# Kernel optimization log

Hardware: AMD Instinct MI355X
Metric: run time of the kernel (lower is better)

## Reference

```python
import jax, jax.numpy as jnp
import numpy as np

NUM_HEADS = 16
HEAD_DIM = 64  # hidden 1024 / 16


def setup_inputs() -> dict:
    key = jax.random.key(0)
    k1, k2, k3 = jax.random.split(key, 3)
    B, S, H = 2, 2048, 1024
    return {
        "hidden_states": jax.random.normal(k1, (B, S, H), dtype=jnp.float32),
        "attention_mask": jnp.zeros((B, 1, 1, S), dtype=jnp.float32),
        "c_attn_w": jax.random.normal(k2, (H, 3 * H), dtype=jnp.float32) * 0.02,
        "c_attn_b": jnp.zeros((3 * H,), dtype=jnp.float32),
        "c_proj_w": jax.random.normal(k3, (H, H), dtype=jnp.float32) * 0.02,
        "c_proj_b": jnp.zeros((H,), dtype=jnp.float32),
    }


def reference(hidden_states, attention_mask, c_attn_w, c_attn_b, c_proj_w, c_proj_b):
    B, S, H = hidden_states.shape
    nH, hd = NUM_HEADS, HEAD_DIM
    # Conv1D: x @ w + b (HF weight layout is (in, out))
    qkv = hidden_states @ c_attn_w + c_attn_b  # [B,S,3H]
    q, k, v = jnp.split(qkv, 3, axis=-1)
    # split heads -> [B,nH,S,hd]
    def heads(t):
        return t.reshape(B, S, nH, hd).transpose(0, 2, 1, 3)
    q, k, v = heads(q), heads(k), heads(v)
    scores = jnp.einsum("bhqd,bhkd->bhqk", q, k) / np.sqrt(hd).astype(jnp.float32)
    scores = scores + attention_mask  # additive mask, broadcast [B,1,1,S]
    attn = jax.nn.softmax(scores, axis=-1)  # dropout is identity (eval)
    ctx = jnp.einsum("bhqk,bhkd->bhqd", attn, v)
    ctx = ctx.transpose(0, 2, 1, 3).reshape(B, S, H)  # merge heads
    out = ctx @ c_proj_w + c_proj_b
    return out
```

## Files before the change

kernel.cpp:

```cpp
#include <hip/hip_runtime.h>
#include <hip/hip_bf16.h>

typedef __attribute__((ext_vector_type(8))) short short8;
typedef __attribute__((ext_vector_type(4))) short short4v;
typedef __attribute__((ext_vector_type(4))) float f32x4;

__device__ __forceinline__ unsigned short f2bf(float f) {
  union { __hip_bfloat16 h; unsigned short u; } cv;
  cv.h = __float2bfloat16(f);
  return cv.u;
}

__device__ __forceinline__ void gld16(const void* g, void* l) {
  __builtin_amdgcn_global_load_lds(
      (const __attribute__((address_space(1))) unsigned int*)g,
      (__attribute__((address_space(3))) unsigned int*)l, 16, 0, 0);
}

__device__ __forceinline__ f32x4 mfma_bf16(short8 a, short8 b, f32x4 c) {
  return __builtin_amdgcn_mfma_f32_16x16x32_bf16(a, b, c, 0, 0, 0);
}

#define QSCALE 0.18033688011112042f
#define L2E    1.4426950408889634f

__global__ void prep(const float* __restrict__ x, unsigned short* __restrict__ xbf,
                     const float* __restrict__ wa, unsigned short* __restrict__ da,
                     const float* __restrict__ wp, unsigned short* __restrict__ dp) {
  __shared__ float tile[64][65];
  const int t = threadIdx.x;
  const int bid = blockIdx.x;
  if (bid < 4096) {
    int i = bid * 256 + t;
    float4 v = ((const float4*)x)[i];
    ushort4 o;
    o.x = f2bf(v.x); o.y = f2bf(v.y); o.z = f2bf(v.z); o.w = f2bf(v.w);
    ((ushort4*)xbf)[i] = o;
    return;
  }
  int idx = bid - 4096;
  const int tr = idx & 15;
  int y = idx >> 4;
  const float* src;
  unsigned short* dst;
  int C;
  if (y < 48) { src = wa; dst = da; C = 3072; }
  else        { src = wp; dst = dp; C = 1024; y -= 48; }
  const int tc = y;
#pragma unroll
  for (int i = 0; i < 16; ++i) {
    int id2 = t + i * 256;
    int lr = id2 >> 6, lc = id2 & 63;
    tile[lr][lc] = src[(size_t)(tr * 64 + lr) * C + tc * 64 + lc];
  }
  __syncthreads();
#pragma unroll
  for (int i = 0; i < 16; ++i) {
    int id2 = t + i * 256;
    int lr = id2 >> 6, lc = id2 & 63;
    dst[(size_t)(tc * 64 + lr) * 1024 + tr * 64 + lc] = f2bf(tile[lc][lr]);
  }
}

template <int KDIM>
__device__ __forceinline__ void gemm_core(const short* __restrict__ A, const short* __restrict__ Bt,
                                          int mbase, int nbase, short* As, short* Bs,
                                          int wm, int wn, int quad, int l16, int t,
                                          f32x4 (&acc)[4][4]) {
  for (int kt = 0; kt < KDIM / 32; ++kt) {
#pragma unroll
    for (int i = 0; i < 2; ++i) {
      int c = t + i * 256;
      int row = c >> 2, c4 = c & 3;
      gld16(A + (size_t)(mbase + row) * KDIM + kt * 32 + c4 * 8, (char*)As + c * 16);
      gld16(Bt + (size_t)(nbase + row) * KDIM + kt * 32 + c4 * 8, (char*)Bs + c * 16);
    }
    __syncthreads();
    short8 af[4], bf[4];
#pragma unroll
    for (int m = 0; m < 4; ++m)
      af[m] = *(const short8*)((const char*)As + (wm + m * 16 + l16) * 64 + quad * 16);
#pragma unroll
    for (int n = 0; n < 4; ++n)
      bf[n] = *(const short8*)((const char*)Bs + (wn + n * 16 + l16) * 64 + quad * 16);
#pragma unroll
    for (int m = 0; m < 4; ++m)
#pragma unroll
      for (int n = 0; n < 4; ++n)
        acc[m][n] = mfma_bf16(af[m], bf[n], acc[m][n]);
    __syncthreads();
  }
}

__global__ __launch_bounds__(256, 2) void gemm_qkv(
    const short* __restrict__ A, const short* __restrict__ Bt, const float* __restrict__ bias,
    unsigned short* __restrict__ q, unsigned short* __restrict__ k,
    unsigned short* __restrict__ vt) {
  __shared__ __align__(16) char smem[17408];
  short* As = (short*)smem;
  short* Bs = (short*)(smem + 8192);
  unsigned short* vlds = (unsigned short*)smem;
  const int t = threadIdx.x;
  const int wave = t >> 6, lane = t & 63;
  const int quad = lane >> 4, l16 = lane & 15;
  const int wm = (wave >> 1) * 64, wn = (wave & 1) * 64;
  const int mbase = blockIdx.x * 128, nbase = blockIdx.y * 128;
  f32x4 acc[4][4];
#pragma unroll
  for (int i = 0; i < 4; ++i)
#pragma unroll
    for (int j = 0; j < 4; ++j) acc[i][j] = (f32x4)0.0f;
  gemm_core<1024>(A, Bt, mbase, nbase, As, Bs, wm, wn, quad, l16, t, acc);

  if (nbase < 2048) {
#pragma unroll
    for (int n = 0; n < 4; ++n) {
      int col = nbase + wn + n * 16 + l16;
      float bc = bias[col];
      int which = col >> 10, rem = col & 1023;
      int h = rem >> 6, d = rem & 63;
      unsigned short* dst = which ? k : q;
      float scale = which ? 1.0f : QSCALE;
#pragma unroll
      for (int m = 0; m < 4; ++m) {
#pragma unroll
        for (int r = 0; r < 4; ++r) {
          int row = mbase + wm + m * 16 + quad * 4 + r;
          int b = row >> 11, s = row & 2047;
          dst[(((size_t)(b * 16 + h)) * 2048 + s) * 64 + d] = f2bf((acc[m][n][r] + bc) * scale);
        }
      }
    }
  } else {
    const int b = mbase >> 11, s0 = mbase & 2047;
    const int vcb = nbase - 2048;
    __syncthreads();
#pragma unroll
    for (int half = 0; half < 2; ++half) {
      if (wn == half * 64) {
#pragma unroll
        for (int n = 0; n < 4; ++n) {
          int col_l = n * 16 + l16;
          float bc = bias[nbase + half * 64 + col_l];
#pragma unroll
          for (int m = 0; m < 4; ++m)
#pragma unroll
            for (int r = 0; r < 4; ++r) {
              int row_l = wm + m * 16 + quad * 4 + r;
              int idx = (row_l & 64) + (row_l & 15) * 4 + ((row_l >> 4) & 3);
              vlds[col_l * 136 + idx] = f2bf(acc[m][n][r] + bc);
            }
        }
      }
      __syncthreads();
      int h = (vcb + half * 64) >> 6;
      size_t obase = ((size_t)(b * 16 + h)) * 64 * 2048;
#pragma unroll
      for (int i = 0; i < 4; ++i) {
        int c = t + i * 256;
        int d_l = c >> 4, c16 = c & 15;
        short8 v = *(const short8*)&vlds[d_l * 136 + c16 * 8];
        *(short8*)&vt[obase + (size_t)d_l * 2048 + s0 + c16 * 8] = v;
      }
      __syncthreads();
    }
  }
}

__global__ __launch_bounds__(256, 2) void gemm_proj(
    const short* __restrict__ A, const short* __restrict__ Bt, const float* __restrict__ bias,
    float* __restrict__ out) {
  __shared__ __align__(16) short As[64 * 32];
  __shared__ __align__(16) short Bs[128 * 32];
  const int t = threadIdx.x;
  const int wave = t >> 6, lane = t & 63;
  const int quad = lane >> 4, l16 = lane & 15;
  const int wm = (wave >> 1) * 32, wn = (wave & 1) * 64;
  const int mbase = blockIdx.x * 64, nbase = blockIdx.y * 128;
  f32x4 acc[2][4];
#pragma unroll
  for (int i = 0; i < 2; ++i)
#pragma unroll
    for (int j = 0; j < 4; ++j) acc[i][j] = (f32x4)0.0f;
  for (int kt = 0; kt < 32; ++kt) {
    {
      int row = t >> 2, c4 = t & 3;
      gld16(A + (size_t)(mbase + row) * 1024 + kt * 32 + c4 * 8, (char*)As + t * 16);
    }
#pragma unroll
    for (int i = 0; i < 2; ++i) {
      int c = t + i * 256;
      int row = c >> 2, c4 = c & 3;
      gld16(Bt + (size_t)(nbase + row) * 1024 + kt * 32 + c4 * 8, (char*)Bs + c * 16);
    }
    __syncthreads();
    short8 af[2], bf[4];
#pragma unroll
    for (int m = 0; m < 2; ++m)
      af[m] = *(const short8*)((const char*)As + (wm + m * 16 + l16) * 64 + quad * 16);
#pragma unroll
    for (int n = 0; n < 4; ++n)
      bf[n] = *(const short8*)((const char*)Bs + (wn + n * 16 + l16) * 64 + quad * 16);
#pragma unroll
    for (int m = 0; m < 2; ++m)
#pragma unroll
      for (int n = 0; n < 4; ++n)
        acc[m][n] = mfma_bf16(af[m], bf[n], acc[m][n]);
    __syncthreads();
  }
#pragma unroll
  for (int n = 0; n < 4; ++n) {
    int col = nbase + wn + n * 16 + l16;
    float bc = bias[col];
#pragma unroll
    for (int m = 0; m < 2; ++m)
#pragma unroll
      for (int r = 0; r < 4; ++r) {
        int row = mbase + wm + m * 16 + quad * 4 + r;
        out[(size_t)row * 1024 + col] = acc[m][n][r] + bc;
      }
  }
}

__global__ __launch_bounds__(256, 4) void flash_attn(
    const short* __restrict__ Qg, const short* __restrict__ Kg, const short* __restrict__ Vtg,
    const float* __restrict__ mask, unsigned short* __restrict__ ctx) {
  __shared__ __align__(16) unsigned char smem[40960];
  short* Psm = (short*)(smem + 32768);
  const int t = threadIdx.x;
  const int wave = t >> 6, lane = t & 63;
  const int quad = lane >> 4, l16 = lane & 15;
  const int bh = blockIdx.x, b = bh >> 4, h = bh & 15;
  const int qbase = blockIdx.y * 64;
  const size_t bh_off = (size_t)bh * 2048 * 64;

#pragma unroll
  for (int i = 0; i < 2; ++i) {
    int c = t + i * 256;
    int row = c >> 3, col = c & 7;
    gld16(Qg + bh_off + (size_t)(qbase + row) * 64 + (col ^ (row & 7)) * 8,
          (char*)smem + c * 16);
  }
  __syncthreads();
  short8 qf[2];
#pragma unroll
  for (int ks = 0; ks < 2; ++ks) {
    int row = wave * 16 + l16;
    qf[ks] = *(const short8*)((const char*)smem +
                              (row * 8 + ((ks * 4 + quad) ^ (l16 & 7))) * 16);
  }
  __syncthreads();

  auto stage = [&](int kn) {
    char* kd = (char*)smem + (kn & 1) * 8192;
    char* vd = (char*)smem + 16384 + (kn & 1) * 8192;
#pragma unroll
    for (int i = 0; i < 2; ++i) {
      int c = t + i * 256;
      int row = c >> 3, col = c & 7;
      gld16(Kg + bh_off + (size_t)(kn * 64 + row) * 64 + (col ^ (row & 7)) * 8,
            kd + c * 16);
      gld16(Vtg + ((size_t)bh * 64 + row) * 2048 + kn * 64 + (col ^ (row & 7)) * 8,
            vd + c * 16);
    }
  };

  f32x4 O[4];
  float l_i[4];
#pragma unroll
  for (int d = 0; d < 4; ++d) O[d] = (f32x4)0.0f;
#pragma unroll
  for (int r = 0; r < 4; ++r) l_i[r] = 0.0f;

  stage(0);
  __syncthreads();

  for (int kt = 0; kt < 32; ++kt) {
    const char* Kc = (const char*)smem + (kt & 1) * 8192;
    const char* Vc = (const char*)smem + 16384 + (kt & 1) * 8192;

    float mv[4];
#pragma unroll
    for (int n = 0; n < 4; ++n) mv[n] = mask[b * 2048 + kt * 64 + n * 16 + l16];

    if (kt < 31) stage(kt + 1);

    f32x4 sa[4];
#pragma unroll
    for (int n = 0; n < 4; ++n) sa[n] = (f32x4)0.0f;
    __builtin_amdgcn_s_setprio(1);
#pragma unroll
    for (int ks = 0; ks < 2; ++ks) {
#pragma unroll
      for (int n = 0; n < 4; ++n) {
        int row = n * 16 + l16;
        short8 kf = *(const short8*)(Kc + (row * 8 + ((ks * 4 + quad) ^ (l16 & 7))) * 16);
        sa[n] = mfma_bf16(qf[ks], kf, sa[n]);
      }
    }
    __builtin_amdgcn_s_setprio(0);

#pragma unroll
    for (int r = 0; r < 4; ++r) {
      float rs = 0.0f;
      short4v p4;
#pragma unroll
      for (int n = 0; n < 4; ++n) {
        float p = __builtin_amdgcn_exp2f(__builtin_fmaf(mv[n], L2E, sa[n][r]));
        rs += p;
        p4[n] = (short)f2bf(p);
      }
      int prow = wave * 16 + quad * 4 + r;
      *(short4v*)((char*)Psm + prow * 128 +
                  (((l16 >> 1) ^ (prow & 7)) * 16) + (l16 & 1) * 8) = p4;
      l_i[r] += rs;
    }
    asm volatile("" ::: "memory");

    __builtin_amdgcn_s_setprio(1);
#pragma unroll
    for (int ks = 0; ks < 2; ++ks) {
      int u = ks * 4 + quad;
      int prow = wave * 16 + l16;
      short8 pf = *(const short8*)((const char*)Psm + prow * 128 + ((u ^ (l16 & 7)) * 16));
#pragma unroll
      for (int db = 0; db < 4; ++db) {
        int d = db * 16 + l16;
        short8 vf = *(const short8*)(Vc + d * 128 + ((u ^ (d & 7)) * 16));
        O[db] = mfma_bf16(pf, vf, O[db]);
      }
    }
    __builtin_amdgcn_s_setprio(0);

    __syncthreads();
  }

#pragma unroll
  for (int r = 0; r < 4; ++r) {
    float l = l_i[r];
    l += __shfl_xor(l, 1);
    l += __shfl_xor(l, 2);
    l += __shfl_xor(l, 4);
    l += __shfl_xor(l, 8);
    float inv = 1.0f / l;
    int s = qbase + wave * 16 + quad * 4 + r;
    size_t o = ((size_t)b * 2048 + s) * 1024 + h * 64;
#pragma unroll
    for (int db = 0; db < 4; ++db)
      ctx[o + db * 16 + l16] = f2bf(O[db][r] * inv);
  }
}

extern "C" void kernel_launch(void* const* d_in, const int* in_sizes, int n_in,
                              void* d_out, int out_size, void* d_ws, size_t ws_size,
                              hipStream_t stream) {
  const float* x      = (const float*)d_in[0];
  const float* mask   = (const float*)d_in[1];
  const float* w_attn = (const float*)d_in[2];
  const float* b_attn = (const float*)d_in[3];
  const float* w_proj = (const float*)d_in[4];
  const float* b_proj = (const float*)d_in[5];
  float* out = (float*)d_out;

  char* ws = (char*)d_ws;
  const size_t MB = 1024 * 1024;
  short*          Xbf    = (short*)(ws);
  short*          Wqkv_t = (short*)(ws + 8 * MB);
  short*          Wprj_t = (short*)(ws + 14 * MB);
  unsigned short* Qb     = (unsigned short*)(ws + 16 * MB);
  unsigned short* Kb     = (unsigned short*)(ws + 24 * MB);
  unsigned short* Vtb    = (unsigned short*)(ws + 32 * MB);
  unsigned short* ctx    = (unsigned short*)Xbf;

  prep<<<5120, 256, 0, stream>>>(x, (unsigned short*)Xbf,
                                 w_attn, (unsigned short*)Wqkv_t,
                                 w_proj, (unsigned short*)Wprj_t);
  gemm_qkv<<<dim3(32, 24), 256, 0, stream>>>(Xbf, Wqkv_t, b_attn, Qb, Kb, Vtb);
  flash_attn<<<dim3(32, 32), 256, 0, stream>>>((const short*)Qb, (const short*)Kb,
                                               (const short*)Vtb, mask, ctx);
  gemm_proj<<<dim3(64, 8), 256, 0, stream>>>((const short*)ctx, Wprj_t, b_proj, out);
}
```

Baseline: 188.7 us.

## Process 128 query rows per flash-attention block to reuse K/V tiles

Each flash-attention block now handles 128 query rows instead of 64, with every wave computing two 16-row MFMA fragments. Each K and V fragment loaded from LDS then feeds two MFMAs, and the grid is halved, so each K/V tile is fetched from global memory half as often. In exchange the block uses more registers and more LDS (48KB), launch bounds drop occupancy to 2 blocks per CU, and only 512 blocks are launched, which gives less latency hiding.

```diff
diff --git a/kernel.cpp b/kernel.cpp
--- a/kernel.cpp
+++ b/kernel.cpp
@@ -222,33 +222,35 @@
   }
 }
 
-__global__ __launch_bounds__(256, 4) void flash_attn(
+__global__ __launch_bounds__(256, 2) void flash_attn(
     const short* __restrict__ Qg, const short* __restrict__ Kg, const short* __restrict__ Vtg,
     const float* __restrict__ mask, unsigned short* __restrict__ ctx) {
-  __shared__ __align__(16) unsigned char smem[40960];
+  __shared__ __align__(16) unsigned char smem[49152];
   short* Psm = (short*)(smem + 32768);
   const int t = threadIdx.x;
   const int wave = t >> 6, lane = t & 63;
   const int quad = lane >> 4, l16 = lane & 15;
   const int bh = blockIdx.x, b = bh >> 4, h = bh & 15;
-  const int qbase = blockIdx.y * 64;
+  const int qbase = blockIdx.y * 128;
   const size_t bh_off = (size_t)bh * 2048 * 64;
 
 #pragma unroll
-  for (int i = 0; i < 2; ++i) {
+  for (int i = 0; i < 4; ++i) {
     int c = t + i * 256;
     int row = c >> 3, col = c & 7;
     gld16(Qg + bh_off + (size_t)(qbase + row) * 64 + (col ^ (row & 7)) * 8,
           (char*)smem + c * 16);
   }
   __syncthreads();
-  short8 qf[2];
-#pragma unroll
-  for (int ks = 0; ks < 2; ++ks) {
-    int row = wave * 16 + l16;
-    qf[ks] = *(const short8*)((const char*)smem +
-                              (row * 8 + ((ks * 4 + quad) ^ (l16 & 7))) * 16);
-  }
+  short8 qf[2][2];
+#pragma unroll
+  for (int mf = 0; mf < 2; ++mf)
+#pragma unroll
+    for (int ks = 0; ks < 2; ++ks) {
+      int row = wave * 32 + mf * 16 + l16;
+      qf[mf][ks] = *(const short8*)((const char*)smem +
+                                    (row * 8 + ((ks * 4 + quad) ^ (l16 & 7))) * 16);
+    }
   __syncthreads();
 
   auto stage = [&](int kn) {
@@ -265,12 +267,16 @@
     }
   };
 
-  f32x4 O[4];
-  float l_i[4];
-#pragma unroll
-  for (int d = 0; d < 4; ++d) O[d] = (f32x4)0.0f;
-#pragma unroll
-  for (int r = 0; r < 4; ++r) l_i[r] = 0.0f;
+  f32x4 O[2][4];
+  float l_i[2][4];
+#pragma unroll
+  for (int mf = 0; mf < 2; ++mf)
+#pragma unroll
+    for (int d = 0; d < 4; ++d) O[mf][d] = (f32x4)0.0f;
+#pragma unroll
+  for (int mf = 0; mf < 2; ++mf)
+#pragma unroll
+    for (int r = 0; r < 4; ++r) l_i[mf][r] = 0.0f;
 
   stage(0);
   __syncthreads();
@@ -285,9 +291,11 @@
 
     if (kt < 31) stage(kt + 1);
 
-    f32x4 sa[4];
-#pragma unroll
-    for (int n = 0; n < 4; ++n) sa[n] = (f32x4)0.0f;
+    f32x4 sa[2][4];
+#pragma unroll
+    for (int mf = 0; mf < 2; ++mf)
+#pragma unroll
+      for (int n = 0; n < 4; ++n) sa[mf][n] = (f32x4)0.0f;
     __builtin_amdgcn_s_setprio(1);
 #pragma unroll
     for (int ks = 0; ks < 2; ++ks) {
@@ -295,25 +303,29 @@
       for (int n = 0; n < 4; ++n) {
         int row = n * 16 + l16;
         short8 kf = *(const short8*)(Kc + (row * 8 + ((ks * 4 + quad) ^ (l16 & 7))) * 16);
-        sa[n] = mfma_bf16(qf[ks], kf, sa[n]);
+        sa[0][n] = mfma_bf16(qf[0][ks], kf, sa[0][n]);
+        sa[1][n] = mfma_bf16(qf[1][ks], kf, sa[1][n]);
       }
     }
     __builtin_amdgcn_s_setprio(0);
 
 #pragma unroll
-    for (int r = 0; r < 4; ++r) {
-      float rs = 0.0f;
-      short4v p4;
-#pragma unroll
-      for (int n = 0; n < 4; ++n) {
-        float p = __builtin_amdgcn_exp2f(__builtin_fmaf(mv[n], L2E, sa[n][r]));
-        rs += p;
-        p4[n] = (short)f2bf(p);
-      }
-      int prow = wave * 16 + quad * 4 + r;
-      *(short4v*)((char*)Psm + prow * 128 +
-                  (((l16 >> 1) ^ (prow & 7)) * 16) + (l16 & 1) * 8) = p4;
-      l_i[r] += rs;
+    for (int mf = 0; mf < 2; ++mf) {
+#pragma unroll
+      for (int r = 0; r < 4; ++r) {
+        float rs = 0.0f;
+        short4v p4;
+#pragma unroll
+        for (int n = 0; n < 4; ++n) {
+          float p = __builtin_amdgcn_exp2f(__builtin_fmaf(mv[n], L2E, sa[mf][n][r]));
+          rs += p;
+          p4[n] = (short)f2bf(p);
+        }
+        int prow = wave * 32 + mf * 16 + quad * 4 + r;
+        *(short4v*)((char*)Psm + prow * 128 +
+                    (((l16 >> 1) ^ (prow & 7)) * 16) + (l16 & 1) * 8) = p4;
+        l_i[mf][r] += rs;
+      }
     }
     asm volatile("" ::: "memory");
 
@@ -321,13 +333,19 @@
 #pragma unroll
     for (int ks = 0; ks < 2; ++ks) {
       int u = ks * 4 + quad;
-      int prow = wave * 16 + l16;
-      short8 pf = *(const short8*)((const char*)Psm + prow * 128 + ((u ^ (l16 & 7)) * 16));
+      short8 vf[4];
 #pragma unroll
       for (int db = 0; db < 4; ++db) {
         int d = db * 16 + l16;
-        short8 vf = *(const short8*)(Vc + d * 128 + ((u ^ (d & 7)) * 16));
-        O[db] = mfma_bf16(pf, vf, O[db]);
+        vf[db] = *(const short8*)(Vc + d * 128 + ((u ^ (d & 7)) * 16));
+      }
+#pragma unroll
+      for (int mf = 0; mf < 2; ++mf) {
+        int prow = wave * 32 + mf * 16 + l16;
+        short8 pf = *(const short8*)((const char*)Psm + prow * 128 + ((u ^ (l16 & 7)) * 16));
+#pragma unroll
+        for (int db = 0; db < 4; ++db)
+          O[mf][db] = mfma_bf16(pf, vf[db], O[mf][db]);
       }
     }
     __builtin_amdgcn_s_setprio(0);
@@ -336,18 +354,21 @@
   }
 
 #pragma unroll
-  for (int r = 0; r < 4; ++r) {
-    float l = l_i[r];
-    l += __shfl_xor(l, 1);
-    l += __shfl_xor(l, 2);
-    l += __shfl_xor(l, 4);
-    l += __shfl_xor(l, 8);
-    float inv = 1.0f / l;
-    int s = qbase + wave * 16 + quad * 4 + r;
-    size_t o = ((size_t)b * 2048 + s) * 1024 + h * 64;
-#pragma unroll
-    for (int db = 0; db < 4; ++db)
-      ctx[o + db * 16 + l16] = f2bf(O[db][r] * inv);
+  for (int mf = 0; mf < 2; ++mf) {
+#pragma unroll
+    for (int r = 0; r < 4; ++r) {
+      float l = l_i[mf][r];
+      l += __shfl_xor(l, 1);
+      l += __shfl_xor(l, 2);
+      l += __shfl_xor(l, 4);
+      l += __shfl_xor(l, 8);
+      float inv = 1.0f / l;
+      int s = qbase + wave * 32 + mf * 16 + quad * 4 + r;
+      size_t o = ((size_t)b * 2048 + s) * 1024 + h * 64;
+#pragma unroll
+      for (int db = 0; db < 4; ++db)
+        ctx[o + db * 16 + l16] = f2bf(O[mf][db][r] * inv);
+    }
   }
 }
 
@@ -376,7 +397,7 @@
                                  w_attn, (unsigned short*)Wqkv_t,
                                  w_proj, (unsigned short*)Wprj_t);
   gemm_qkv<<<dim3(32, 24), 256, 0, stream>>>(Xbf, Wqkv_t, b_attn, Qb, Kb, Vtb);
-  flash_attn<<<dim3(32, 32), 256, 0, stream>>>((const short*)Qb, (const short*)Kb,
+  flash_attn<<<dim3(32, 16), 256, 0, stream>>>((const short*)Qb, (const short*)Kb,
                                                (const short*)Vtb, mask, ctx);
   gemm_proj<<<dim3(64, 8), 256, 0, stream>>>((const short*)ctx, Wprj_t, b_proj, out);
 }
```

Measured after the change: 184.5 us. 1.02x faster.
